# Optimization experiments

Hardware: AMD Instinct MI355X
Metric: run time of the kernel (lower is better)

## Reference

```python
import jax, jax.numpy as jnp
import numpy as np
from jax import lax

T, B, C = 50, 50, 4096
PADLEN = 49
ORDER = 2
BANDS = [(0.05, 0.15), (0.2, 0.4)]


def _butter_bandpass_sos(n, w1, w2):
    """Butterworth bandpass design (scipy.signal.iirfilter(..., ftype='butter', output='sos') equivalent)."""
    fs = 2.0
    warped = 2.0 * fs * np.tan(np.pi * np.array([w1, w2]) / fs)  # pre-warped analog freqs
    bw = warped[1] - warped[0]
    wo = np.sqrt(warped[0] * warped[1])
    k = np.arange(1, n + 1)
    p = -np.exp(1j * np.pi * (2 * k - 1) / (2 * n))  # analog LP prototype poles
    # lp2bp: n poles -> 2n poles, n zeros at origin, gain *= bw**n
    p_lp = p * bw / 2.0
    disc = np.sqrt(p_lp ** 2 - wo ** 2 + 0j)
    p_bp = np.concatenate([p_lp + disc, p_lp - disc])
    # bilinear transform (fs=2): zeros at origin -> +1; n zeros at infinity -> -1
    fs2 = 2.0 * fs
    p_d = (fs2 + p_bp) / (fs2 - p_bp)
    gain = (bw ** n) * (fs2 ** n) / np.real(np.prod(fs2 - p_bp))
    # pair conjugate poles into biquads; numerator (z-1)(z+1) = [1, 0, -1]
    pos = p_d[np.imag(p_d) > 0]
    assert len(pos) == n, 'expected complex-conjugate pole pairs'
    sos = []
    for i, pp in enumerate(pos):
        a = np.array([1.0, -2.0 * np.real(pp), np.abs(pp) ** 2])
        b = np.array([1.0, 0.0, -1.0])
        if i == 0:
            b = b * gain
        sos.append(np.concatenate([b, a]))
    return np.array(sos)  # [n_sections, 6]


def _sosfilt_zi(sos):
    """scipy.signal.sosfilt_zi: steady-state per-section initial conditions (DF2T)."""
    n_sections = sos.shape[0]
    zi = np.zeros((n_sections, 2))
    scale = 1.0
    for s in range(n_sections):
        b, a = sos[s, :3], sos[s, 3:]
        B0 = b[1] - a[1] * b[0]
        B1 = b[2] - a[2] * b[0]
        det = 1.0 + a[1] + a[2]
        zi[s, 0] = scale * (B0 + B1) / det
        zi[s, 1] = scale * ((1.0 + a[1]) * B1 - a[2] * B0) / det
        scale *= b.sum() / a.sum()
    return zi


def _sosfilt(sos, x, zi):
    """Cascaded biquads, direct form II transposed, scan over time axis 0.
    x: [T, B, C]; zi: list of (z0, z1) each [B, C]."""
    y = x
    for s in range(sos.shape[0]):
        b0, b1, b2 = (float(sos[s, 0]), float(sos[s, 1]), float(sos[s, 2]))
        a1, a2 = float(sos[s, 4]), float(sos[s, 5])
        def step(carry, xt, b0=b0, b1=b1, b2=b2, a1=a1, a2=a2):
            z0, z1 = carry
            yt = b0 * xt + z0
            return (b1 * xt + z1 - a1 * yt, b2 * xt - a2 * yt), yt
        _, y = lax.scan(step, (zi[s][0], zi[s][1]), y)
    return y


def _odd_ext(x, n):
    left = 2.0 * x[0] - x[n:0:-1]
    right = 2.0 * x[-1] - x[-2:-n - 2:-1]
    return jnp.concatenate([left, x, right], axis=0)


def _sosfiltfilt(sos, x, padlen):
    zi = _sosfilt_zi(sos)  # [S, 2] numpy
    ext = _odd_ext(x, padlen)  # [T + 2*padlen, B, C]
    x0 = ext[0]
    zi_f = [(float(zi[s, 0]) * x0, float(zi[s, 1]) * x0) for s in range(sos.shape[0])]
    y = _sosfilt(sos, ext, zi_f)
    y = y[::-1]
    y0 = y[0]
    zi_b = [(float(zi[s, 0]) * y0, float(zi[s, 1]) * y0) for s in range(sos.shape[0])]
    y = _sosfilt(sos, y, zi_b)
    y = y[::-1]
    return y[padlen:-padlen]


def _tensor_zscore(x):
    # Faithful to the original expand([50,-1,-1]).permute(1,0,2) quirk:
    # mean/std over axis 0 give [B, C]; the permute aligns them with the TIME axis,
    # i.e. out[t, b, c] = (x[t, b, c] - m[t, c]) / s[t, c]  (valid since T == B == 50).
    m = x.mean(axis=0)
    s = x.std(axis=0, ddof=1)  # torch.std default is unbiased
    return (x - m[:, None, :]) / s[:, None, :]


def setup_inputs() -> dict:
    key = jax.random.key(0)
    sample = jax.random.normal(key, (T, B, C), dtype=jnp.float32)
    return {"sample": sample}


def reference(sample):
    outs = []
    for (w1, w2) in BANDS:
        sos = _butter_bandpass_sos(ORDER, w1, w2)
        y = _sosfiltfilt(sos, sample, PADLEN)
        y = y - y.mean(axis=0)  # bandpass branch: mean-center
        y = _tensor_zscore(y)   # normalize=True
        outs.append(y)
    return jnp.stack(outs)  # [n_bands, T, B, C]
```

## Files before the change

kernel.cpp:

```cpp
#include <hip/hip_runtime.h>
#include <cmath>
#include <complex>

constexpr int TT  = 50;
constexpr int NB  = 50;
constexpr int NC  = 4096;
constexpr int NCH = NB * NC;
constexpr int PAD = 49;
constexpr int EXT = TT + 2 * PAD;
constexpr int BS  = 256;

struct Coefs {
    double b0[2][2], b1[2][2], b2[2][2], a1[2][2], a2[2][2];
    double zi0[2][2], zi1[2][2];
};

__global__ void __launch_bounds__(64) build_M(float* __restrict__ Mt, Coefs cf) {
    __shared__ double e[EXT][TT];
    const int band = blockIdx.x;
    const int j = threadIdx.x;
    if (j >= TT) return;

    const double b0a = cf.b0[band][0], b1a = cf.b1[band][0], b2a = cf.b2[band][0];
    const double a1a = cf.a1[band][0], a2a = cf.a2[band][0];
    const double b0b = cf.b0[band][1], b1b = cf.b1[band][1], b2b = cf.b2[band][1];
    const double a1b = cf.a1[band][1], a2b = cf.a2[band][1];

    const double x0 = (j == 0 ? 2.0 : 0.0) - (j == PAD ? 1.0 : 0.0);

    double za0 = cf.zi0[band][0] * x0, za1 = cf.zi1[band][0] * x0;
    double zb0 = cf.zi0[band][1] * x0, zb1 = cf.zi1[band][1] * x0;

    double ylast = 0.0;
#pragma unroll
    for (int i = 0; i < EXT; ++i) {
        double xt;
        if (i < PAD) {
            xt = (j == 0 ? 2.0 : 0.0) - (j == (PAD - i) ? 1.0 : 0.0);
        } else if (i < PAD + TT) {
            xt = (j == (i - PAD) ? 1.0 : 0.0);
        } else {
            xt = (j == TT - 1 ? 2.0 : 0.0) - (j == (2 * TT - 2 + PAD - i) ? 1.0 : 0.0);
        }
        const double y0 = b0a * xt + za0;
        za0 = b1a * xt + za1 - a1a * y0;
        za1 = b2a * xt - a2a * y0;
        const double y1 = b0b * y0 + zb0;
        zb0 = b1b * y0 + zb1 - a1b * y1;
        zb1 = b2b * y0 - a2b * y1;
        e[i][j] = y1;
        ylast = y1;
    }

    za0 = cf.zi0[band][0] * ylast; za1 = cf.zi1[band][0] * ylast;
    zb0 = cf.zi0[band][1] * ylast; zb1 = cf.zi1[band][1] * ylast;
#pragma unroll 4
    for (int m = 0; m < EXT; ++m) {
        const int i = EXT - 1 - m;
        const double xt = e[i][j];
        const double y0 = b0a * xt + za0;
        za0 = b1a * xt + za1 - a1a * y0;
        za1 = b2a * xt - a2a * y0;
        const double y1 = b0b * y0 + zb0;
        zb0 = b1b * y0 + zb1 - a1b * y1;
        zb1 = b2b * y0 - a2b * y1;
        e[i][j] = y1;
    }

    double mean = 0.0;
#pragma unroll
    for (int t = 0; t < TT; ++t) mean += e[PAD + t][j];
    mean *= (1.0 / TT);
#pragma unroll
    for (int t = 0; t < TT; ++t)
        Mt[(band * TT + j) * TT + t] = (float)(e[PAD + t][j] - mean);
}

__device__ __forceinline__ void column_gemv(float (&f)[TT],
                                            const float* __restrict__ xcol,
                                            const float* __restrict__ Mb) {
#pragma unroll
    for (int t = 0; t < TT; ++t) f[t] = 0.f;
#pragma unroll 5
    for (int k = 0; k < TT; ++k) {
        const float xk = xcol[(size_t)k * NCH];
        const float* __restrict__ r = Mb + k * TT;
#pragma unroll
        for (int t = 0; t < TT; ++t) f[t] = fmaf(r[t], xk, f[t]);
    }
}

__global__ __launch_bounds__(BS) __attribute__((amdgpu_waves_per_eu(1, 4)))
void stats_kern(const float* __restrict__ x, const float* __restrict__ Mt,
                float* __restrict__ stats) {
    const int id   = blockIdx.x * BS + threadIdx.x;
    const int band = blockIdx.y;

    float f[TT];
    column_gemv(f, x + id, Mt + band * (TT * TT));

    float mu = 0.f;
#pragma unroll
    for (int t = 0; t < TT; ++t) mu += f[t];
    mu *= (1.0f / TT);
    float ss = 0.f;
#pragma unroll
    for (int t = 0; t < TT; ++t) {
        const float h = f[t] - mu;
        ss = fmaf(h, h, ss);
    }
    const float inv = 1.0f / sqrtf(ss * (1.0f / (TT - 1)));

    float* __restrict__ sb = stats + (size_t)band * 2 * NCH;
    sb[id]        = mu;
    sb[NCH + id]  = inv;
}

__global__ __launch_bounds__(BS) __attribute__((amdgpu_waves_per_eu(1, 4)))
void norm_kern(const float* __restrict__ x, const float* __restrict__ Mt,
               const float* __restrict__ stats, float* __restrict__ out) {
    const int id   = blockIdx.x * BS + threadIdx.x;
    const int band = blockIdx.y;
    const int c    = id & (NC - 1);

    float f[TT];
    column_gemv(f, x + id, Mt + band * (TT * TT));

    const float* __restrict__ mu_b  = stats + (size_t)band * 2 * NCH;
    const float* __restrict__ inv_b = mu_b + NCH;
    float* __restrict__ ob = out + (size_t)band * TT * NCH;

#pragma unroll
    for (int t = 0; t < TT; ++t) {
        const float m = mu_b[(size_t)t * NC + c];
        const float s = inv_b[(size_t)t * NC + c];
        ob[(size_t)t * NCH + id] = (f[t] - m) * s;
    }
}

static Coefs make_coefs() {
    Coefs cf;
    const double bands[2][2] = {{0.05, 0.15}, {0.2, 0.4}};
    const int n = 2;
    for (int bd = 0; bd < 2; ++bd) {
        const double fs = 2.0;
        const double w1 = bands[bd][0], w2 = bands[bd][1];
        const double warped0 = 2.0 * fs * std::tan(M_PI * w1 / fs);
        const double warped1 = 2.0 * fs * std::tan(M_PI * w2 / fs);
        const double bw = warped1 - warped0;
        const double wo = std::sqrt(warped0 * warped1);
        std::complex<double> p_bp[4];
        for (int k = 1; k <= n; ++k) {
            std::complex<double> p = -std::exp(std::complex<double>(0.0, M_PI * (2 * k - 1) / (2.0 * n)));
            std::complex<double> plp = p * (bw / 2.0);
            std::complex<double> disc = std::sqrt(plp * plp - std::complex<double>(wo * wo, 0.0));
            p_bp[k - 1] = plp + disc;
            p_bp[n + k - 1] = plp - disc;
        }
        const double fs2 = 2.0 * fs;
        std::complex<double> prod(1.0, 0.0);
        for (int i = 0; i < 2 * n; ++i) prod *= (fs2 - p_bp[i]);
        const double gain = std::pow(bw, n) * std::pow(fs2, n) / prod.real();
        std::complex<double> p_d[4];
        for (int i = 0; i < 2 * n; ++i) p_d[i] = (fs2 + p_bp[i]) / (fs2 - p_bp[i]);
        double sos[2][6];
        int cnt = 0;
        for (int i = 0; i < 2 * n; ++i) {
            if (p_d[i].imag() > 0) {
                const double g = (cnt == 0) ? gain : 1.0;
                sos[cnt][0] = g;
                sos[cnt][1] = 0.0;
                sos[cnt][2] = -g;
                sos[cnt][3] = 1.0;
                sos[cnt][4] = -2.0 * p_d[i].real();
                sos[cnt][5] = std::norm(p_d[i]);
                ++cnt;
            }
        }
        double scale = 1.0;
        for (int s = 0; s < 2; ++s) {
            const double b0 = sos[s][0], b1 = sos[s][1], b2 = sos[s][2];
            const double a1 = sos[s][4], a2 = sos[s][5];
            const double B0 = b1 - a1 * b0, B1 = b2 - a2 * b0;
            const double det = 1.0 + a1 + a2;
            cf.b0[bd][s] = b0; cf.b1[bd][s] = b1; cf.b2[bd][s] = b2;
            cf.a1[bd][s] = a1; cf.a2[bd][s] = a2;
            cf.zi0[bd][s] = scale * (B0 + B1) / det;
            cf.zi1[bd][s] = scale * ((1.0 + a1) * B1 - a2 * B0) / det;
            scale *= (b0 + b1 + b2) / (1.0 + a1 + a2);
        }
    }
    return cf;
}

extern "C" void kernel_launch(void* const* d_in, const int* in_sizes, int n_in,
                              void* d_out, int out_size, void* d_ws, size_t ws_size,
                              hipStream_t stream) {
    const float* x = (const float*)d_in[0];
    float* out = (float*)d_out;
    float* Mt = (float*)d_ws;
    float* stats = Mt + 8192;

    const Coefs cf = make_coefs();
    build_M<<<dim3(2), dim3(64), 0, stream>>>(Mt, cf);
    stats_kern<<<dim3(NCH / BS, 2), dim3(BS), 0, stream>>>(x, Mt, stats);
    norm_kern <<<dim3(NCH / BS, 2), dim3(BS), 0, stream>>>(x, Mt, stats, out);
}
```

Before: 181.0 us.

## Fuse stats and normalize kernels via per-block shared-memory stats over batch

Replaces the separate stats and normalize kernels, which each recomputed the filtering GEMV, with one kernel. Each block covers 16 channels across all 50 batch rows, so the per-(b,c) mean and inverse std that normalization indexes by t can be exchanged through shared memory. This removes the duplicate GEMV, the second read of the input and the stats round-trip through global memory. In exchange it adds a block-wide barrier, and the 800-thread blocks with large register arrays may lower occupancy. Coalescing also shrinks to 16-wide segments.

```diff
diff --git a/kernel.cpp b/kernel.cpp
--- a/kernel.cpp
+++ b/kernel.cpp
@@ -8,7 +8,7 @@
 constexpr int NCH = NB * NC;
 constexpr int PAD = 49;
 constexpr int EXT = TT + 2 * PAD;
-constexpr int BS  = 256;
+constexpr int CT  = 16;
 
 struct Coefs {
     double b0[2][2], b1[2][2], b2[2][2], a1[2][2], a2[2][2];
@@ -76,11 +76,25 @@
         Mt[(band * TT + j) * TT + t] = (float)(e[PAD + t][j] - mean);
 }
 
-__device__ __forceinline__ void column_gemv(float (&f)[TT],
-                                            const float* __restrict__ xcol,
-                                            const float* __restrict__ Mb) {
+__global__ __launch_bounds__(CT * NB) __attribute__((amdgpu_waves_per_eu(1, 4)))
+void fused_bn(const float* __restrict__ x, const float* __restrict__ Mt,
+              float* __restrict__ out) {
+    const int tx   = threadIdx.x;
+    const int b    = threadIdx.y;
+    const int band = blockIdx.y;
+    const int c    = blockIdx.x * CT + tx;
+    const int i    = b * NC + c;
+
+    __shared__ float sm_mu [NB][CT];
+    __shared__ float sm_inv[NB][CT];
+
+    const float* __restrict__ Mb   = Mt + band * (TT * TT);
+    const float* __restrict__ xcol = x + i;
+
+    float f[TT];
 #pragma unroll
     for (int t = 0; t < TT; ++t) f[t] = 0.f;
+
 #pragma unroll 5
     for (int k = 0; k < TT; ++k) {
         const float xk = xcol[(size_t)k * NCH];
@@ -88,16 +102,6 @@
 #pragma unroll
         for (int t = 0; t < TT; ++t) f[t] = fmaf(r[t], xk, f[t]);
     }
-}
-
-__global__ __launch_bounds__(BS) __attribute__((amdgpu_waves_per_eu(1, 4)))
-void stats_kern(const float* __restrict__ x, const float* __restrict__ Mt,
-                float* __restrict__ stats) {
-    const int id   = blockIdx.x * BS + threadIdx.x;
-    const int band = blockIdx.y;
-
-    float f[TT];
-    column_gemv(f, x + id, Mt + band * (TT * TT));
 
     float mu = 0.f;
 #pragma unroll
@@ -111,30 +115,15 @@
     }
     const float inv = 1.0f / sqrtf(ss * (1.0f / (TT - 1)));
 
-    float* __restrict__ sb = stats + (size_t)band * 2 * NCH;
-    sb[id]        = mu;
-    sb[NCH + id]  = inv;
-}
+    sm_mu [b][tx] = mu;
+    sm_inv[b][tx] = inv;
+    __syncthreads();
 
-__global__ __launch_bounds__(BS) __attribute__((amdgpu_waves_per_eu(1, 4)))
-void norm_kern(const float* __restrict__ x, const float* __restrict__ Mt,
-               const float* __restrict__ stats, float* __restrict__ out) {
-    const int id   = blockIdx.x * BS + threadIdx.x;
-    const int band = blockIdx.y;
-    const int c    = id & (NC - 1);
-
-    float f[TT];
-    column_gemv(f, x + id, Mt + band * (TT * TT));
-
-    const float* __restrict__ mu_b  = stats + (size_t)band * 2 * NCH;
-    const float* __restrict__ inv_b = mu_b + NCH;
     float* __restrict__ ob = out + (size_t)band * TT * NCH;
-
 #pragma unroll
     for (int t = 0; t < TT; ++t) {
-        const float m = mu_b[(size_t)t * NC + c];
-        const float s = inv_b[(size_t)t * NC + c];
-        ob[(size_t)t * NCH + id] = (f[t] - m) * s;
+        const float v = (f[t] - sm_mu[t][tx]) * sm_inv[t][tx];
+        ob[(size_t)t * NCH + i] = v;
     }
 }
 
@@ -199,10 +188,8 @@
     const float* x = (const float*)d_in[0];
     float* out = (float*)d_out;
     float* Mt = (float*)d_ws;
-    float* stats = Mt + 8192;
 
     const Coefs cf = make_coefs();
     build_M<<<dim3(2), dim3(64), 0, stream>>>(Mt, cf);
-    stats_kern<<<dim3(NCH / BS, 2), dim3(BS), 0, stream>>>(x, Mt, stats);
-    norm_kern <<<dim3(NCH / BS, 2), dim3(BS), 0, stream>>>(x, Mt, stats, out);
+    fused_bn<<<dim3(NC / CT, 2), dim3(CT, NB), 0, stream>>>(x, Mt, out);
 }
```

Result: faster. 153.4 us (-15.3%).
